# Kernel tuning notes

Hardware: AMD Instinct MI355X
Metric: run time of the kernel (lower is better)

Reference implementation:

```python
import jax, jax.numpy as jnp
import numpy as np

N_NODES = 10000
N_EDGES = 320000
HIDDEN = 256
HEADS = 8
HEAD_DIM = HIDDEN // HEADS  # 32
NEG_SLOPE = 0.2


def setup_inputs() -> dict:
    key = jax.random.key(0)
    ks = jax.random.split(key, 12)
    x = jax.random.normal(ks[0], (N_NODES, HIDDEN), dtype=jnp.float32)
    edges_idx = jax.random.randint(ks[1], (2, N_EDGES), 0, N_NODES, dtype=jnp.int64)
    s = 1.0 / np.sqrt(HIDDEN)
    # layer 1 params
    W1 = jax.random.normal(ks[2], (HIDDEN, HEADS * HEAD_DIM), dtype=jnp.float32) * s
    a_src1 = jax.random.normal(ks[3], (HEADS, HEAD_DIM), dtype=jnp.float32) * s
    a_dst1 = jax.random.normal(ks[4], (HEADS, HEAD_DIM), dtype=jnp.float32) * s
    b1 = jnp.zeros((HEADS * HEAD_DIM,), dtype=jnp.float32)
    # layer 2 params
    W2 = jax.random.normal(ks[5], (HIDDEN, HEADS * HEAD_DIM), dtype=jnp.float32) * s
    a_src2 = jax.random.normal(ks[6], (HEADS, HEAD_DIM), dtype=jnp.float32) * s
    a_dst2 = jax.random.normal(ks[7], (HEADS, HEAD_DIM), dtype=jnp.float32) * s
    b2 = jnp.zeros((HEADS * HEAD_DIM,), dtype=jnp.float32)
    return {"x": x, "edges_idx": edges_idx,
            "W1": W1, "a_src1": a_src1, "a_dst1": a_dst1, "b1": b1,
            "W2": W2, "a_src2": a_src2, "a_dst2": a_dst2, "b2": b2}


def gat_conv(x, src, dst, W, a_src, a_dst, b):
    """PyG GATConv (concat=True, negative_slope=0.2), dropout in eval mode."""
    N = x.shape[0]
    h = (x @ W).reshape(N, HEADS, HEAD_DIM)          # [N,H,C]
    alpha_s = jnp.einsum('nhc,hc->nh', h, a_src)     # [N,H]
    alpha_d = jnp.einsum('nhc,hc->nh', h, a_dst)     # [N,H]
    e = alpha_s[src] + alpha_d[dst]                  # [E,H]
    e = jnp.where(e > 0, e, NEG_SLOPE * e)           # leaky_relu
    # scatter-softmax over incoming edges of each dst node
    m = jax.ops.segment_max(e, dst, num_segments=N)  # [N,H]
    ex = jnp.exp(e - m[dst])                         # [E,H]
    denom = jax.ops.segment_sum(ex, dst, num_segments=N)  # [N,H]
    alpha = ex / (denom[dst] + 1e-16)                # [E,H]
    msg = h[src] * alpha[:, :, None]                 # [E,H,C]
    out = jax.ops.segment_sum(msg, dst, num_segments=N)   # [N,H,C]
    return out.reshape(N, HEADS * HEAD_DIM) + b


def reference(x, edges_idx, W1, a_src1, a_dst1, b1, W2, a_src2, a_dst2, b2):
    src = edges_idx[0]
    dst = edges_idx[1]
    h = gat_conv(x, src, dst, W1, a_src1, a_dst1, b1)
    h = jax.nn.elu(h)
    out = gat_conv(h, src, dst, W2, a_src2, a_dst2, b2)
    return out
```

## Files before the change

kernel.cpp:

```cpp
#include <hip/hip_runtime.h>
#include <hip/hip_bf16.h>
#include <hip/hip_fp16.h>

#define N_NODES 10000
#define N_EDGES 320000
#define HIDDEN 256
#define HEADS 8
#define HEAD_DIM 32
#define NEG_SLOPE 0.2f
#define CAP 80

typedef __attribute__((ext_vector_type(8))) short short8;
typedef __attribute__((ext_vector_type(8))) _Float16 half8;
typedef __attribute__((ext_vector_type(4))) float f32x4;

__device__ __forceinline__ void bf16_split(float v, unsigned short& hi, unsigned short& lo) {
    __hip_bfloat16 hb = __float2bfloat16(v);
    float hf = __bfloat162float(hb);
    __hip_bfloat16 lb = __float2bfloat16(v - hf);
    hi = *reinterpret_cast<unsigned short*>(&hb);
    lo = *reinterpret_cast<unsigned short*>(&lb);
}

__global__ __launch_bounds__(256) void prep_kernel(
    const float* __restrict__ W1, const float* __restrict__ W2,
    const int* __restrict__ src, const int* __restrict__ dst,
    unsigned short* __restrict__ w1h, unsigned short* __restrict__ w1l,
    unsigned short* __restrict__ w2h, unsigned short* __restrict__ w2l,
    int* __restrict__ counts, int* __restrict__ csr_src) {
    int b = blockIdx.x;
    int tid = threadIdx.x;
    if (b < 512) {
        int i = b * 256 + tid;
        int which = i >> 16;
        int rem = i & 0xFFFF;
        int k = rem >> 8, n = rem & 255;
        const float* W = which ? W2 : W1;
        unsigned short* wh = which ? w2h : w1h;
        unsigned short* wl = which ? w2l : w1l;
        unsigned short h, l;
        bf16_split(W[k * 256 + n], h, l);
        wh[n * 256 + k] = h;
        wl[n * 256 + k] = l;
    } else {
        int e = (b - 512) * 256 + tid;
        int d = dst[e];
        int rank = atomicAdd(&counts[d], 1);
        csr_src[d * CAP + rank] = src[e];
    }
}

template <int AFP32>
__global__ __launch_bounds__(512) void gemm_mfma_kernel(
    const float* __restrict__ Axf,
    const unsigned short* __restrict__ Ah, const unsigned short* __restrict__ Al,
    const unsigned short* __restrict__ BhT, const unsigned short* __restrict__ BlT,
    _Float16* __restrict__ hH, const float* __restrict__ a_src,
    const float* __restrict__ a_dst, float* __restrict__ alpha_s,
    float* __restrict__ alpha_d) {
    __shared__ __align__(16) char smem[160768];
    unsigned short* sAh0 = (unsigned short*)smem;
    unsigned short* sAl0 = (unsigned short*)(smem + 6400);
    unsigned short* sAh1 = (unsigned short*)(smem + 12800);
    unsigned short* sAl1 = (unsigned short*)(smem + 19200);
    unsigned short* sBh  = (unsigned short*)(smem + 25600);
    unsigned short* sBl  = (unsigned short*)(smem + 93184);
    _Float16* sOut = (_Float16*)(smem + 25600);

    const int tid = threadIdx.x;
    const int w = tid >> 6, lane = tid & 63;
    const int c = w & 3, g = w >> 2;
    const int rtbase = g ? 3 : 0, nrt = g ? 2 : 3;
    const int col = lane & 15, quad = lane >> 4;
    const int m0 = blockIdx.y * 80, n0 = blockIdx.x * 128;

    f32x4 acc[3][2] = {};
    float4 raf[4][2];
    uint4 rau[4][2];

#define LOAD_A(k0, SS)                                                          \
    if (AFP32) {                                                                \
        _Pragma("unroll") for (int i = 0; i < 2; ++i) {                         \
            int t = tid + i * 512;                                              \
            if (t < 640) {                                                      \
                int row = t >> 3, seg = t & 7;                                  \
                raf[SS][i] = *(const float4*)&Axf[(size_t)(m0 + row) * 256 + (k0) + seg * 4]; \
            }                                                                   \
        }                                                                       \
    } else {                                                                    \
        _Pragma("unroll") for (int i = 0; i < 2; ++i) {                         \
            int t = tid + i * 512;                                              \
            if (t < 640) {                                                      \
                int tt = t < 320 ? t : t - 320;                                 \
                int row = tt >> 2, seg = tt & 3;                                \
                const unsigned short* P = t < 320 ? Ah : Al;                    \
                rau[SS][i] = *(const uint4*)&P[(size_t)(m0 + row) * 256 + (k0) + seg * 8]; \
            }                                                                   \
        }                                                                       \
    }
#define WRITE_A(SS, BUF)                                                        \
    {                                                                           \
        unsigned short* dh_ = (BUF) ? sAh1 : sAh0;                              \
        unsigned short* dl_ = (BUF) ? sAl1 : sAl0;                              \
        if (AFP32) {                                                            \
            _Pragma("unroll") for (int i = 0; i < 2; ++i) {                     \
                int t = tid + i * 512;                                          \
                if (t < 640) {                                                  \
                    int row = t >> 3, seg = t & 7;                              \
                    float4 v = raf[SS][i];                                      \
                    ushort4 hh, ll;                                             \
                    unsigned short hb, lb;                                      \
                    bf16_split(v.x, hb, lb); hh.x = hb; ll.x = lb;              \
                    bf16_split(v.y, hb, lb); hh.y = hb; ll.y = lb;              \
                    bf16_split(v.z, hb, lb); hh.z = hb; ll.z = lb;              \
                    bf16_split(v.w, hb, lb); hh.w = hb; ll.w = lb;              \
                    *(ushort4*)&dh_[row * 40 + seg * 4] = hh;                   \
                    *(ushort4*)&dl_[row * 40 + seg * 4] = ll;                   \
                }                                                               \
            }                                                                   \
        } else {                                                                \
            _Pragma("unroll") for (int i = 0; i < 2; ++i) {                     \
                int t = tid + i * 512;                                          \
                if (t < 640) {                                                  \
                    int tt = t < 320 ? t : t - 320;                             \
                    int row = tt >> 2, seg = tt & 3;                            \
                    unsigned short* Sp = t < 320 ? dh_ : dl_;                   \
                    *(uint4*)&Sp[row * 40 + seg * 8] = rau[SS][i];              \
                }                                                               \
            }                                                                   \
        }                                                                       \
    }
#define COMPUTE(ks)                                                             \
    {                                                                           \
        const unsigned short* ah_ = ((ks) & 1) ? sAh1 : sAh0;                   \
        const unsigned short* al_ = ((ks) & 1) ? sAl1 : sAl0;                   \
        const int kb = (ks) * 32 + quad * 8;                                    \
        short8 bh0 = *(const short8*)&sBh[(c * 32 + col) * 264 + kb];           \
        short8 bl0 = *(const short8*)&sBl[(c * 32 + col) * 264 + kb];           \
        short8 bh1 = *(const short8*)&sBh[(c * 32 + 16 + col) * 264 + kb];      \
        short8 bl1 = *(const short8*)&sBl[(c * 32 + 16 + col) * 264 + kb];      \
        _Pragma("unroll") for (int rt = 0; rt < 3; ++rt) {                      \
            if (rt < nrt) {                                                     \
                int rg = rtbase + rt;                                           \
                short8 ah = *(const short8*)&ah_[(rg * 16 + col) * 40 + quad * 8]; \
                short8 al = *(const short8*)&al_[(rg * 16 + col) * 40 + quad * 8]; \
                acc[rt][0] = __builtin_amdgcn_mfma_f32_16x16x32_bf16(ah, bh0, acc[rt][0], 0, 0, 0); \
                acc[rt][0] = __builtin_amdgcn_mfma_f32_16x16x32_bf16(ah, bl0, acc[rt][0], 0, 0, 0); \
                acc[rt][0] = __builtin_amdgcn_mfma_f32_16x16x32_bf16(al, bh0, acc[rt][0], 0, 0, 0); \
                acc[rt][1] = __builtin_amdgcn_mfma_f32_16x16x32_bf16(ah, bh1, acc[rt][1], 0, 0, 0); \
                acc[rt][1] = __builtin_amdgcn_mfma_f32_16x16x32_bf16(ah, bl1, acc[rt][1], 0, 0, 0); \
                acc[rt][1] = __builtin_amdgcn_mfma_f32_16x16x32_bf16(al, bh1, acc[rt][1], 0, 0, 0); \
            }                                                                   \
        }                                                                       \
    }

    LOAD_A(0, 0)
    LOAD_A(32, 1)
    LOAD_A(64, 2)
    LOAD_A(96, 3)

    WRITE_A(0, 0)
    LOAD_A(128, 0)

    {
        uint4 rbh[8], rbl[8];
#pragma unroll
        for (int i = 0; i < 8; ++i) {
            int chunk = tid + i * 512;
            int row = chunk >> 5, ks8 = chunk & 31;
            rbh[i] = *(const uint4*)&BhT[(size_t)(n0 + row) * 256 + ks8 * 8];
            rbl[i] = *(const uint4*)&BlT[(size_t)(n0 + row) * 256 + ks8 * 8];
        }
#pragma unroll
        for (int i = 0; i < 8; ++i) {
            int chunk = tid + i * 512;
            int row = chunk >> 5, ks8 = chunk & 31;
            *(uint4*)&sBh[row * 264 + ks8 * 8] = rbh[i];
            *(uint4*)&sBl[row * 264 + ks8 * 8] = rbl[i];
        }
    }
    __syncthreads();

#define STEP(ks, REFILL)                                                        \
    WRITE_A((ks + 1) & 3, (ks + 1) & 1)                                         \
    if (REFILL) { LOAD_A((ks + 5) * 32, (ks + 1) & 3) }                         \
    COMPUTE(ks)                                                                 \
    __syncthreads();

    STEP(0, 1)
    STEP(1, 1)
    STEP(2, 1)
    STEP(3, 0)
    STEP(4, 0)
    STEP(5, 0)
    STEP(6, 0)
    COMPUTE(7)
    __syncthreads();
#undef STEP
#undef LOAD_A
#undef WRITE_A
#undef COMPUTE

    const int head = blockIdx.x * 4 + c;
    float as0 = a_src[n0 + c * 32 + col];
    float as1 = a_src[n0 + c * 32 + 16 + col];
    float ad0 = a_dst[n0 + c * 32 + col];
    float ad1 = a_dst[n0 + c * 32 + 16 + col];
#pragma unroll
    for (int rt = 0; rt < 3; ++rt) {
        if (rt < nrt) {
            int rg = rtbase + rt;
#pragma unroll
            for (int r = 0; r < 4; ++r) {
                int row = rg * 16 + quad * 4 + r;
                sOut[row * 264 + c * 32 + col]      = (_Float16)acc[rt][0][r];
                sOut[row * 264 + c * 32 + 16 + col] = (_Float16)acc[rt][1][r];
                float ps = acc[rt][0][r] * as0 + acc[rt][1][r] * as1;
                float pd = acc[rt][0][r] * ad0 + acc[rt][1][r] * ad1;
#pragma unroll
                for (int m = 1; m < 16; m <<= 1) {
                    ps += __shfl_xor(ps, m);
                    pd += __shfl_xor(pd, m);
                }
                if (col == 0) {
                    int gm = m0 + row;
                    alpha_s[gm * HEADS + head] = ps;
                    alpha_d[gm * HEADS + head] = pd;
                }
            }
        }
    }
    __syncthreads();
#pragma unroll
    for (int i = 0; i < 3; ++i) {
        int t = tid + i * 512;
        if (t < 1280) {
            int row = t >> 4, seg = t & 15;
            *(half8*)&hH[(size_t)(m0 + row) * 256 + n0 + seg * 8] =
                *(const half8*)&sOut[row * 264 + seg * 8];
        }
    }
}

__global__ __launch_bounds__(256) void aggregate_kernel(
    const int* __restrict__ counts, const int* __restrict__ csr_src,
    const float* __restrict__ alpha_s, const float* __restrict__ alpha_d,
    const _Float16* __restrict__ hH, const float* __restrict__ bias,
    float* __restrict__ outf, unsigned short* __restrict__ oh,
    unsigned short* __restrict__ ol, int mode) {
    const int tid = threadIdx.x;
    const int w = tid >> 6, lane = tid & 63;
    const int d = blockIdx.x * 4 + w;
    const int q = lane >> 4, fl = lane & 15;
    const int hd0 = fl >> 2, hd1 = 4 + (fl >> 2);
    const int qb = q * 4;
    const int* __restrict__ bucket = csr_src + d * CAP;
    const _Float16* hp0 = hH + fl * 8;
    const _Float16* hp1 = hH + 128 + fl * 8;

    const int n = counts[d];
    const float ad0 = alpha_d[d * HEADS + hd0];
    const float ad1 = alpha_d[d * HEADS + hd1];
    int4 s0_ = *(const int4*)&bucket[qb];
    int4 s1_ = *(const int4*)&bucket[qb + 16];
    int4 s2_ = *(const int4*)&bucket[qb + 32];
    int4 s3_ = *(const int4*)&bucket[qb + 48];

    float accA[8] = {}, accB[8] = {};
    float denA = 0.f, denB = 0.f;

#define AGG_DECL(t) float aA##t##0, aA##t##1, aA##t##2, aA##t##3;               \
                    float aB##t##0, aB##t##1, aB##t##2, aB##t##3;               \
                    half8 hA##t##0, hA##t##1, hA##t##2, hA##t##3;               \
                    half8 hB##t##0, hB##t##1, hB##t##2, hB##t##3;
    AGG_DECL(0) AGG_DECL(1) AGG_DECL(2) AGG_DECL(3) AGG_DECL(4)

#define AGG_CLAMP(x) ((x) < 0 ? 0 : ((x) > 9999 ? 9999 : (x)))
#define AGG_GATHER(t, sv)                                                       \
    {                                                                           \
        int i0_ = AGG_CLAMP((sv).x), i1_ = AGG_CLAMP((sv).y);                   \
        int i2_ = AGG_CLAMP((sv).z), i3_ = AGG_CLAMP((sv).w);                   \
        aA##t##0 = alpha_s[i0_ * HEADS + hd0];                                  \
        aA##t##1 = alpha_s[i1_ * HEADS + hd0];                                  \
        aA##t##2 = alpha_s[i2_ * HEADS + hd0];                                  \
        aA##t##3 = alpha_s[i3_ * HEADS + hd0];                                  \
        aB##t##0 = alpha_s[i0_ * HEADS + hd1];                                  \
        aB##t##1 = alpha_s[i1_ * HEADS + hd1];                                  \
        aB##t##2 = alpha_s[i2_ * HEADS + hd1];                                  \
        aB##t##3 = alpha_s[i3_ * HEADS + hd1];                                  \
        hA##t##0 = *(const half8*)&hp0[(size_t)i0_ * HIDDEN];                   \
        hA##t##1 = *(const half8*)&hp0[(size_t)i1_ * HIDDEN];                   \
        hA##t##2 = *(const half8*)&hp0[(size_t)i2_ * HIDDEN];                   \
        hA##t##3 = *(const half8*)&hp0[(size_t)i3_ * HIDDEN];                   \
        hB##t##0 = *(const half8*)&hp1[(size_t)i0_ * HIDDEN];                   \
        hB##t##1 = *(const half8*)&hp1[(size_t)i1_ * HIDDEN];                   \
        hB##t##2 = *(const half8*)&hp1[(size_t)i2_ * HIDDEN];                   \
        hB##t##3 = *(const half8*)&hp1[(size_t)i3_ * HIDDEN];                   \
    }
#define AGG_COMPUTE(t, base)                                                    \
    {                                                                           \
        int b0_ = (base) + qb;                                                  \
        float eA0 = aA##t##0 + ad0; eA0 = eA0 > 0.f ? eA0 : NEG_SLOPE * eA0;    \
        float eA1 = aA##t##1 + ad0; eA1 = eA1 > 0.f ? eA1 : NEG_SLOPE * eA1;    \
        float eA2 = aA##t##2 + ad0; eA2 = eA2 > 0.f ? eA2 : NEG_SLOPE * eA2;    \
        float eA3 = aA##t##3 + ad0; eA3 = eA3 > 0.f ? eA3 : NEG_SLOPE * eA3;    \
        float eB0 = aB##t##0 + ad1; eB0 = eB0 > 0.f ? eB0 : NEG_SLOPE * eB0;    \
        float eB1 = aB##t##1 + ad1; eB1 = eB1 > 0.f ? eB1 : NEG_SLOPE * eB1;    \
        float eB2 = aB##t##2 + ad1; eB2 = eB2 > 0.f ? eB2 : NEG_SLOPE * eB2;    \
        float eB3 = aB##t##3 + ad1; eB3 = eB3 > 0.f ? eB3 : NEG_SLOPE * eB3;    \
        if (b0_ >= n)     { eA0 = -1e30f; eB0 = -1e30f; }                       \
        if (b0_ + 1 >= n) { eA1 = -1e30f; eB1 = -1e30f; }                       \
        if (b0_ + 2 >= n) { eA2 = -1e30f; eB2 = -1e30f; }                       \
        if (b0_ + 3 >= n) { eA3 = -1e30f; eB3 = -1e30f; }                       \
        float vA0 = __expf(eA0), vA1 = __expf(eA1);                             \
        float vA2 = __expf(eA2), vA3 = __expf(eA3);                             \
        float vB0 = __expf(eB0), vB1 = __expf(eB1);                             \
        float vB2 = __expf(eB2), vB3 = __expf(eB3);                             \
        denA += (vA0 + vA1) + (vA2 + vA3);                                      \
        denB += (vB0 + vB1) + (vB2 + vB3);                                      \
        _Pragma("unroll") for (int j = 0; j < 8; ++j)                           \
            accA[j] += (float)hA##t##0[j] * vA0 + (float)hA##t##1[j] * vA1 +    \
                       (float)hA##t##2[j] * vA2 + (float)hA##t##3[j] * vA3;     \
        _Pragma("unroll") for (int j = 0; j < 8; ++j)                           \
            accB[j] += (float)hB##t##0[j] * vB0 + (float)hB##t##1[j] * vB1 +    \
                       (float)hB##t##2[j] * vB2 + (float)hB##t##3[j] * vB3;     \
    }

    if (n > 0)  AGG_GATHER(0, s0_)
    if (n > 16) AGG_GATHER(1, s1_)
    if (n > 0)  AGG_COMPUTE(0, 0)
    if (n > 32) AGG_GATHER(2, s2_)
    if (n > 16) AGG_COMPUTE(1, 16)
    if (n > 48) AGG_GATHER(3, s3_)
    if (n > 32) AGG_COMPUTE(2, 32)
    if (n > 48) AGG_COMPUTE(3, 48)
    if (n > 64) {
        int4 s4_ = *(const int4*)&bucket[qb + 64];
        AGG_GATHER(4, s4_)
        AGG_COMPUTE(4, 64)
    }

#undef AGG_DECL
#undef AGG_CLAMP
#undef AGG_GATHER
#undef AGG_COMPUTE

#pragma unroll
    for (int j = 0; j < 8; ++j) {
        accA[j] += __shfl_xor(accA[j], 16);
        accB[j] += __shfl_xor(accB[j], 16);
    }
    denA += __shfl_xor(denA, 16);
    denB += __shfl_xor(denB, 16);
#pragma unroll
    for (int j = 0; j < 8; ++j) {
        accA[j] += __shfl_xor(accA[j], 32);
        accB[j] += __shfl_xor(accB[j], 32);
    }
    denA += __shfl_xor(denA, 32);
    denB += __shfl_xor(denB, 32);

    if (q == 0) {
        float invA = 1.f / (denA + 1e-16f);
        float invB = 1.f / (denB + 1e-16f);
        float vA[8], vB[8];
#pragma unroll
        for (int j = 0; j < 8; ++j) {
            vA[j] = accA[j] * invA + bias[fl * 8 + j];
            vB[j] = accB[j] * invB + bias[128 + fl * 8 + j];
        }
        size_t o0 = (size_t)d * HIDDEN + fl * 8;
        size_t o1 = o0 + 128;
        if (mode == 1) {
            unsigned short hb[8], lb[8];
#pragma unroll
            for (int j = 0; j < 8; ++j) {
                vA[j] = vA[j] > 0.f ? vA[j] : (__expf(vA[j]) - 1.f);
                bf16_split(vA[j], hb[j], lb[j]);
            }
            *(ushort4*)&oh[o0]     = make_ushort4(hb[0], hb[1], hb[2], hb[3]);
            *(ushort4*)&oh[o0 + 4] = make_ushort4(hb[4], hb[5], hb[6], hb[7]);
            *(ushort4*)&ol[o0]     = make_ushort4(lb[0], lb[1], lb[2], lb[3]);
            *(ushort4*)&ol[o0 + 4] = make_ushort4(lb[4], lb[5], lb[6], lb[7]);
#pragma unroll
            for (int j = 0; j < 8; ++j) {
                vB[j] = vB[j] > 0.f ? vB[j] : (__expf(vB[j]) - 1.f);
                bf16_split(vB[j], hb[j], lb[j]);
            }
            *(ushort4*)&oh[o1]     = make_ushort4(hb[0], hb[1], hb[2], hb[3]);
            *(ushort4*)&oh[o1 + 4] = make_ushort4(hb[4], hb[5], hb[6], hb[7]);
            *(ushort4*)&ol[o1]     = make_ushort4(lb[0], lb[1], lb[2], lb[3]);
            *(ushort4*)&ol[o1 + 4] = make_ushort4(lb[4], lb[5], lb[6], lb[7]);
        } else {
            *(float4*)&outf[o0]     = make_float4(vA[0], vA[1], vA[2], vA[3]);
            *(float4*)&outf[o0 + 4] = make_float4(vA[4], vA[5], vA[6], vA[7]);
            *(float4*)&outf[o1]     = make_float4(vB[0], vB[1], vB[2], vB[3]);
            *(float4*)&outf[o1 + 4] = make_float4(vB[4], vB[5], vB[6], vB[7]);
        }
    }
}

extern "C" void kernel_launch(void* const* d_in, const int* in_sizes, int n_in,
                              void* d_out, int out_size, void* d_ws, size_t ws_size,
                              hipStream_t stream) {
    const float* x      = (const float*)d_in[0];
    const int*   edges  = (const int*)d_in[1];
    const float* W1     = (const float*)d_in[2];
    const float* as1    = (const float*)d_in[3];
    const float* ad1    = (const float*)d_in[4];
    const float* b1     = (const float*)d_in[5];
    const float* W2     = (const float*)d_in[6];
    const float* as2    = (const float*)d_in[7];
    const float* ad2    = (const float*)d_in[8];
    const float* b2     = (const float*)d_in[9];
    float* out = (float*)d_out;

    const int* src = edges;
    const int* dst = edges + N_EDGES;

    const size_t NF = (size_t)N_NODES * HIDDEN;
    const size_t NH = (size_t)N_NODES * HEADS;

    char* base = (char*)d_ws;
    _Float16* hH = (_Float16*)base;             base += NF * 2;
    unsigned short* x2h = (unsigned short*)base; base += NF * 2;
    unsigned short* x2l = (unsigned short*)base; base += NF * 2;
    float* alpha_s = (float*)base;              base += NH * 4;
    float* alpha_d = (float*)base;              base += NH * 4;
    unsigned short* w1h = (unsigned short*)base; base += 65536 * 2;
    unsigned short* w1l = (unsigned short*)base; base += 65536 * 2;
    unsigned short* w2h = (unsigned short*)base; base += 65536 * 2;
    unsigned short* w2l = (unsigned short*)base; base += 65536 * 2;
    int* csr_src = (int*)base;                  base += (size_t)N_NODES * CAP * 4;
    int* counts  = (int*)base;                  base += (size_t)N_NODES * 4;

    dim3 gemm_grid(2, 125);
    const int EB = (N_EDGES + 255) / 256;
    const int AGG_B = 2500;

    hipMemsetAsync(counts, 0, N_NODES * sizeof(int), stream);
    prep_kernel<<<512 + EB, 256, 0, stream>>>(W1, W2, src, dst,
                                              w1h, w1l, w2h, w2l, counts, csr_src);

    gemm_mfma_kernel<1><<<gemm_grid, 512, 0, stream>>>(
        x, nullptr, nullptr, w1h, w1l, hH, as1, ad1, alpha_s, alpha_d);
    aggregate_kernel<<<AGG_B, 256, 0, stream>>>(counts, csr_src, alpha_s, alpha_d,
                                                hH, b1, nullptr, x2h, x2l, 1);

    gemm_mfma_kernel<0><<<gemm_grid, 512, 0, stream>>>(
        nullptr, x2h, x2l, w2h, w2l, hH, as2, ad2, alpha_s, alpha_d);
    aggregate_kernel<<<AGG_B, 256, 0, stream>>>(counts, csr_src, alpha_s, alpha_d,
                                                hH, b2, out, nullptr, nullptr, 0);
}
```

Baseline: 180.1 us.

## Fuse weight prep, CSR build and first GEMM into one kernel

Removes the separate prep kernel. The layer-1 GEMM now reads fp32 W1 directly and does the bf16 hi/lo split while loading B into shared memory. A single fused launch runs the layer-1 GEMM blocks, a tiled W2 transpose-split through shared memory, and the CSR bucket build as separate block ranges. This saves one launch and one dependency boundary and lets the GEMM overlap with the atomic CSR fill, at the cost of strided uncoalesced W1 loads repeated in every GEMM block.

```diff
diff --git a/kernel.cpp b/kernel.cpp
--- a/kernel.cpp
+++ b/kernel.cpp
@@ -22,43 +22,16 @@
     lo = *reinterpret_cast<unsigned short*>(&lb);
 }
 
-__global__ __launch_bounds__(256) void prep_kernel(
-    const float* __restrict__ W1, const float* __restrict__ W2,
-    const int* __restrict__ src, const int* __restrict__ dst,
-    unsigned short* __restrict__ w1h, unsigned short* __restrict__ w1l,
-    unsigned short* __restrict__ w2h, unsigned short* __restrict__ w2l,
-    int* __restrict__ counts, int* __restrict__ csr_src) {
-    int b = blockIdx.x;
-    int tid = threadIdx.x;
-    if (b < 512) {
-        int i = b * 256 + tid;
-        int which = i >> 16;
-        int rem = i & 0xFFFF;
-        int k = rem >> 8, n = rem & 255;
-        const float* W = which ? W2 : W1;
-        unsigned short* wh = which ? w2h : w1h;
-        unsigned short* wl = which ? w2l : w1l;
-        unsigned short h, l;
-        bf16_split(W[k * 256 + n], h, l);
-        wh[n * 256 + k] = h;
-        wl[n * 256 + k] = l;
-    } else {
-        int e = (b - 512) * 256 + tid;
-        int d = dst[e];
-        int rank = atomicAdd(&counts[d], 1);
-        csr_src[d * CAP + rank] = src[e];
-    }
-}
-
-template <int AFP32>
-__global__ __launch_bounds__(512) void gemm_mfma_kernel(
+template <int AFP32, int BFP32>
+__device__ __forceinline__ void gemm_body(
+    char* smem, int bx, int by, int tid,
     const float* __restrict__ Axf,
     const unsigned short* __restrict__ Ah, const unsigned short* __restrict__ Al,
+    const float* __restrict__ Wf,
     const unsigned short* __restrict__ BhT, const unsigned short* __restrict__ BlT,
     _Float16* __restrict__ hH, const float* __restrict__ a_src,
     const float* __restrict__ a_dst, float* __restrict__ alpha_s,
     float* __restrict__ alpha_d) {
-    __shared__ __align__(16) char smem[160768];
     unsigned short* sAh0 = (unsigned short*)smem;
     unsigned short* sAl0 = (unsigned short*)(smem + 6400);
     unsigned short* sAh1 = (unsigned short*)(smem + 12800);
@@ -67,12 +40,11 @@
     unsigned short* sBl  = (unsigned short*)(smem + 93184);
     _Float16* sOut = (_Float16*)(smem + 25600);
 
-    const int tid = threadIdx.x;
     const int w = tid >> 6, lane = tid & 63;
     const int c = w & 3, g = w >> 2;
     const int rtbase = g ? 3 : 0, nrt = g ? 2 : 3;
     const int col = lane & 15, quad = lane >> 4;
-    const int m0 = blockIdx.y * 80, n0 = blockIdx.x * 128;
+    const int m0 = by * 80, n0 = bx * 128;
 
     f32x4 acc[3][2] = {};
     float4 raf[4][2];
@@ -162,7 +134,27 @@
     WRITE_A(0, 0)
     LOAD_A(128, 0)
 
-    {
+    if (BFP32) {
+        const int nn = tid & 127, kq = (tid >> 7) * 64;
+        const float* Wc = &Wf[(size_t)kq * 256 + n0 + nn];
+        unsigned short* dh = &sBh[nn * 264 + kq];
+        unsigned short* dl = &sBl[nn * 264 + kq];
+#pragma unroll
+        for (int j = 0; j < 64; j += 4) {
+            float v0 = Wc[(size_t)(j + 0) * 256];
+            float v1 = Wc[(size_t)(j + 1) * 256];
+            float v2 = Wc[(size_t)(j + 2) * 256];
+            float v3 = Wc[(size_t)(j + 3) * 256];
+            ushort4 hh, ll;
+            unsigned short hb, lb;
+            bf16_split(v0, hb, lb); hh.x = hb; ll.x = lb;
+            bf16_split(v1, hb, lb); hh.y = hb; ll.y = lb;
+            bf16_split(v2, hb, lb); hh.z = hb; ll.z = lb;
+            bf16_split(v3, hb, lb); hh.w = hb; ll.w = lb;
+            *(ushort4*)&dh[j] = hh;
+            *(ushort4*)&dl[j] = ll;
+        }
+    } else {
         uint4 rbh[8], rbl[8];
 #pragma unroll
         for (int i = 0; i < 8; ++i) {
@@ -201,7 +193,7 @@
 #undef WRITE_A
 #undef COMPUTE
 
-    const int head = blockIdx.x * 4 + c;
+    const int head = bx * 4 + c;
     float as0 = a_src[n0 + c * 32 + col];
     float as1 = a_src[n0 + c * 32 + 16 + col];
     float ad0 = a_dst[n0 + c * 32 + col];
@@ -240,6 +232,68 @@
                 *(const half8*)&sOut[row * 264 + seg * 8];
         }
     }
+}
+
+__global__ __launch_bounds__(512) void fused1_kernel(
+    const float* __restrict__ x, const float* __restrict__ W1,
+    const float* __restrict__ W2,
+    const int* __restrict__ src, const int* __restrict__ dst,
+    unsigned short* __restrict__ w2h, unsigned short* __restrict__ w2l,
+    int* __restrict__ counts, int* __restrict__ csr_src,
+    _Float16* __restrict__ hH, const float* __restrict__ as1,
+    const float* __restrict__ ad1, float* __restrict__ alpha_s,
+    float* __restrict__ alpha_d) {
+    __shared__ __align__(16) char smem[160768];
+    const int b = blockIdx.x, tid = threadIdx.x;
+    if (b < 250) {
+        gemm_body<1, 1>(smem, b & 1, b >> 1, tid, x, nullptr, nullptr, W1,
+                        nullptr, nullptr, hH, as1, ad1, alpha_s, alpha_d);
+    } else if (b < 266) {
+        unsigned short (*sh)[66] = (unsigned short(*)[66])smem;
+        unsigned short (*sl)[66] = (unsigned short(*)[66])(smem + 64 * 66 * 2);
+        const int tile = b - 250;
+        const int kt = (tile >> 2) * 64, nt = (tile & 3) * 64;
+        {
+            const int kl = tid >> 3, ns = (tid & 7) * 8;
+#pragma unroll
+            for (int j = 0; j < 8; j += 4) {
+                float4 v = *(const float4*)&W2[(size_t)(kt + kl) * 256 + nt + ns + j];
+                unsigned short h_, l_;
+                bf16_split(v.x, h_, l_); sh[kl][ns + j]     = h_; sl[kl][ns + j]     = l_;
+                bf16_split(v.y, h_, l_); sh[kl][ns + j + 1] = h_; sl[kl][ns + j + 1] = l_;
+                bf16_split(v.z, h_, l_); sh[kl][ns + j + 2] = h_; sl[kl][ns + j + 2] = l_;
+                bf16_split(v.w, h_, l_); sh[kl][ns + j + 3] = h_; sl[kl][ns + j + 3] = l_;
+            }
+        }
+        __syncthreads();
+        {
+            const int nl = tid >> 3, ks = (tid & 7) * 8;
+            unsigned short oh_[8], ol_[8];
+#pragma unroll
+            for (int j = 0; j < 8; ++j) { oh_[j] = sh[ks + j][nl]; ol_[j] = sl[ks + j][nl]; }
+            size_t base = (size_t)(nt + nl) * 256 + kt + ks;
+            *(ushort4*)&w2h[base]     = make_ushort4(oh_[0], oh_[1], oh_[2], oh_[3]);
+            *(ushort4*)&w2h[base + 4] = make_ushort4(oh_[4], oh_[5], oh_[6], oh_[7]);
+            *(ushort4*)&w2l[base]     = make_ushort4(ol_[0], ol_[1], ol_[2], ol_[3]);
+            *(ushort4*)&w2l[base + 4] = make_ushort4(ol_[4], ol_[5], ol_[6], ol_[7]);
+        }
+    } else {
+        int e = (b - 266) * 512 + tid;
+        int d = dst[e];
+        int rank = atomicAdd(&counts[d], 1);
+        csr_src[d * CAP + rank] = src[e];
+    }
+}
+
+__global__ __launch_bounds__(512) void gemm2_kernel(
+    const unsigned short* __restrict__ Ah, const unsigned short* __restrict__ Al,
+    const unsigned short* __restrict__ BhT, const unsigned short* __restrict__ BlT,
+    _Float16* __restrict__ hH, const float* __restrict__ a_src,
+    const float* __restrict__ a_dst, float* __restrict__ alpha_s,
+    float* __restrict__ alpha_d) {
+    __shared__ __align__(16) char smem[160768];
+    gemm_body<0, 0>(smem, blockIdx.x, blockIdx.y, threadIdx.x, nullptr, Ah, Al,
+                    nullptr, BhT, BlT, hH, a_src, a_dst, alpha_s, alpha_d);
 }
 
 __global__ __launch_bounds__(256) void aggregate_kernel(
@@ -427,28 +481,23 @@
     unsigned short* x2l = (unsigned short*)base; base += NF * 2;
     float* alpha_s = (float*)base;              base += NH * 4;
     float* alpha_d = (float*)base;              base += NH * 4;
-    unsigned short* w1h = (unsigned short*)base; base += 65536 * 2;
-    unsigned short* w1l = (unsigned short*)base; base += 65536 * 2;
     unsigned short* w2h = (unsigned short*)base; base += 65536 * 2;
     unsigned short* w2l = (unsigned short*)base; base += 65536 * 2;
     int* csr_src = (int*)base;                  base += (size_t)N_NODES * CAP * 4;
     int* counts  = (int*)base;                  base += (size_t)N_NODES * 4;
 
     dim3 gemm_grid(2, 125);
-    const int EB = (N_EDGES + 255) / 256;
     const int AGG_B = 2500;
+    const int F1_B = 250 + 16 + 625;
 
     hipMemsetAsync(counts, 0, N_NODES * sizeof(int), stream);
-    prep_kernel<<<512 + EB, 256, 0, stream>>>(W1, W2, src, dst,
-                                              w1h, w1l, w2h, w2l, counts, csr_src);
-
-    gemm_mfma_kernel<1><<<gemm_grid, 512, 0, stream>>>(
-        x, nullptr, nullptr, w1h, w1l, hH, as1, ad1, alpha_s, alpha_d);
+    fused1_kernel<<<F1_B, 512, 0, stream>>>(x, W1, W2, src, dst, w2h, w2l,
+                                            counts, csr_src, hH, as1, ad1,
+                                            alpha_s, alpha_d);
     aggregate_kernel<<<AGG_B, 256, 0, stream>>>(counts, csr_src, alpha_s, alpha_d,
                                                 hH, b1, nullptr, x2h, x2l, 1);
-
-    gemm_mfma_kernel<0><<<gemm_grid, 512, 0, stream>>>(
-        nullptr, x2h, x2l, w2h, w2l, hH, as2, ad2, alpha_s, alpha_d);
+    gemm2_kernel<<<gemm_grid, 512, 0, stream>>>(x2h, x2l, w2h, w2l, hH, as2, ad2,
+                                                alpha_s, alpha_d);
     aggregate_kernel<<<AGG_B, 256, 0, stream>>>(counts, csr_src, alpha_s, alpha_d,
                                                 hH, b2, out, nullptr, nullptr, 0);
 }
```

Result: faster. 176.5 us (-2.0%).
